# Optimization experiments

Hardware: AMD Instinct MI355X
Metric: run time of the kernel (lower is better)

The kernel has to match this reference:

```python
import jax, jax.numpy as jnp
import numpy as np

L, N, E, H = 2048, 4, 256, 4
D = E // H  # head_dim


def setup_inputs() -> dict:
    key = jax.random.key(0)
    ks = jax.random.split(key, 8)
    s = 1.0 / np.sqrt(E)
    return {
        "x": jax.random.normal(ks[0], (L, N, E), jnp.float32),
        "pos_emb": jax.random.normal(ks[1], (1, 2 * L - 1, E), jnp.float32),
        "in_proj_w": jax.random.normal(ks[2], (3 * E, E), jnp.float32) * s,
        "in_proj_b": jnp.zeros((3 * E,), jnp.float32),
        "pos_w": jax.random.normal(ks[3], (E, E), jnp.float32) * s,
        "pos_bias_u": jax.random.normal(ks[4], (H, D), jnp.float32) * s,
        "pos_bias_v": jax.random.normal(ks[5], (H, D), jnp.float32) * s,
        "out_proj_w": jax.random.normal(ks[6], (E, E), jnp.float32) * s,
        "out_proj_b": jnp.zeros((E,), jnp.float32),
    }


def _rel_shift(bd):
    # bd: (N, H, L, 2L-1) -> (N, H, L, L); out[...,i,j] = bd[...,i, L-1-i+j]
    l = bd.shape[2]
    idx = (l - 1) - jnp.arange(l)[:, None] + jnp.arange(l)[None, :]  # (L, L)
    return jnp.take_along_axis(bd, idx[None, None, :, :], axis=-1)


def reference(x, pos_emb, in_proj_w, in_proj_b, pos_w, pos_bias_u,
              pos_bias_v, out_proj_w, out_proj_b):
    scaling = 1.0 / jnp.sqrt(jnp.asarray(D, x.dtype))
    qkv = x @ in_proj_w.T + in_proj_b                # (L, N, 3E)
    q, k, v = jnp.split(qkv, 3, axis=-1)
    q = q * scaling
    # (L,N,E) -> (N,H,L,D)
    q = q.reshape(L, N, H, D).transpose(1, 2, 0, 3)
    k = k.reshape(L, N, H, D).transpose(1, 2, 0, 3)
    v = v.reshape(L, N, H, D).transpose(1, 2, 0, 3)
    # positional projection: (1, 2L-1, E) -> (H, 2L-1, D)
    p = (pos_emb @ pos_w.T).reshape(2 * L - 1, H, D).transpose(1, 0, 2)
    q_u = q + pos_bias_u[None, :, None, :]
    q_v = q + pos_bias_v[None, :, None, :]
    matrix_ac = jnp.einsum('bhld,bhsd->bhls', q_u, k)          # (N,H,L,L)
    matrix_bd = jnp.einsum('bhld,hnd->bhln', q_v, p)           # (N,H,L,2L-1)
    matrix_bd = _rel_shift(matrix_bd)                          # (N,H,L,L)
    scores = matrix_ac + matrix_bd
    attn = jax.nn.softmax(scores, axis=-1)
    out = jnp.einsum('bhls,bhsd->bhld', attn, v)               # (N,H,L,D)
    out = out.transpose(2, 0, 1, 3).reshape(L, N, E)
    return out @ out_proj_w.T + out_proj_b
```

## Files before the change

### kernel.cpp

```cpp
#include <hip/hip_runtime.h>
#include <math.h>
#include <stdint.h>


typedef __attribute__((ext_vector_type(8))) _Float16 half8;
typedef __attribute__((ext_vector_type(4))) float f32x4;
typedef unsigned short u16;
typedef unsigned int u32;

namespace {
constexpr int L_SEQ  = 2048;
constexpr int NB     = 4;
constexpr int EMB    = 256;
constexpr int NH     = 4;
constexpr int HD     = 64;
constexpr int P_ROWS = 2 * L_SEQ - 1;
}

__device__ __forceinline__ u16 f2h(float x) {
    _Float16 h = (_Float16)x;
    return __builtin_bit_cast(u16, h);
}
__device__ __forceinline__ u32 pk2(float a, float b) {
    return (u32)f2h(a) | ((u32)f2h(b) << 16);
}

__global__ __launch_bounds__(256, 2) void qkvpos_gemm(
        const float* __restrict__ x, const float* __restrict__ pos_emb,
        const float* __restrict__ in_w, const float* __restrict__ in_b,
        const float* __restrict__ pos_w,
        const float* __restrict__ u_bias, const float* __restrict__ v_bias,
        u16* __restrict__ quB, u16* __restrict__ qvB,
        u16* __restrict__ kB,  u16* __restrict__ vtB, u16* __restrict__ pB) {
    __shared__ __align__(16) u16 ws[64 * 256];
    __shared__ __align__(16) u16 scr[128 * 72];

    const int t    = threadIdx.x;
    const int lane = t & 63;
    const int w    = t >> 6;
    const int il   = lane & 15;
    const int g    = lane >> 4;

    const int logical = (blockIdx.x & 7) * 112 + (blockIdx.x >> 3);
    const bool isQKV = logical < 768;
    int mg, nt;
    const float *Ap, *W, *Wb;
    if (isQKV) { mg = logical / 12; nt = logical % 12; Ap = x;       W = in_w;  Wb = in_b; }
    else       { const int l2 = logical - 768;
                 mg = l2 >> 2;     nt = l2 & 3;      Ap = pos_emb; W = pos_w; Wb = nullptr; }
    const int m0 = mg * 128, n0 = nt * 64;

    {
        const int kc = (t & 31) * 8, rb_ = t >> 5;
        #pragma unroll
        for (int rr = 0; rr < 8; ++rr) {
            const int row = rb_ * 8 + rr;
            const float* wr = &W[(size_t)(n0 + row) * 256 + kc];
            float4 f0 = *(const float4*)&wr[0];
            float4 f1 = *(const float4*)&wr[4];
            *(uint4*)((char*)ws + row * 512 + ((kc * 2) ^ ((row & 7) << 4))) =
                make_uint4(pk2(f0.x, f0.y), pk2(f0.z, f0.w),
                           pk2(f1.x, f1.y), pk2(f1.z, f1.w));
        }
    }

    half8 bf0[8], bf1[8];
    {
        int r0 = m0 + w * 32 + il;
        int r1 = r0 + 16;
        if (!isQKV) { r0 = r0 > 4094 ? 4094 : r0; r1 = r1 > 4094 ? 4094 : r1; }
        const float* a0 = Ap + (size_t)r0 * 256;
        const float* a1 = Ap + (size_t)r1 * 256;
        #pragma unroll
        for (int c = 0; c < 8; ++c) {
            float4 f0 = *(const float4*)&a0[c * 32 + g * 8];
            float4 f1 = *(const float4*)&a0[c * 32 + g * 8 + 4];
            bf0[c] = __builtin_bit_cast(half8,
                make_uint4(pk2(f0.x, f0.y), pk2(f0.z, f0.w),
                           pk2(f1.x, f1.y), pk2(f1.z, f1.w)));
            float4 h0 = *(const float4*)&a1[c * 32 + g * 8];
            float4 h1 = *(const float4*)&a1[c * 32 + g * 8 + 4];
            bf1[c] = __builtin_bit_cast(half8,
                make_uint4(pk2(h0.x, h0.y), pk2(h0.z, h0.w),
                           pk2(h1.x, h1.y), pk2(h1.z, h1.w)));
        }
    }
    __syncthreads();

    f32x4 acc0[4] = {}, acc1[4] = {};
    __builtin_amdgcn_s_setprio(1);
    #pragma unroll
    for (int c = 0; c < 8; ++c) {
        #pragma unroll
        for (int jt = 0; jt < 4; ++jt) {
            const int row = jt * 16 + il;
            half8 af = *(const half8*)((const char*)ws + row * 512 +
                                       ((c * 64 + g * 16) ^ ((row & 7) << 4)));
            acc0[jt] = __builtin_amdgcn_mfma_f32_16x16x32_f16(af, bf0[c], acc0[jt], 0, 0, 0);
            acc1[jt] = __builtin_amdgcn_mfma_f32_16x16x32_f16(af, bf1[c], acc1[jt], 0, 0, 0);
        }
    }
    __builtin_amdgcn_s_setprio(0);

    float av[2][4][4];
    #pragma unroll
    for (int jt = 0; jt < 4; ++jt)
        #pragma unroll
        for (int r = 0; r < 4; ++r) {
            const float bb = Wb ? Wb[n0 + jt * 16 + g * 4 + r] : 0.f;
            av[0][jt][r] = acc0[jt][r] + bb;
            av[1][jt][r] = acc1[jt][r] + bb;
        }

    u16* scrw = scr + w * (32 * 72);
    const int rrd  = lane >> 1;
    const int base = (lane & 1) * 32;

    auto waveStore = [&](u16* dstBase, int hh, float scale, const float* bias,
                         bool qkvLayout) {
        #pragma unroll
        for (int s = 0; s < 2; ++s)
            #pragma unroll
            for (int jt = 0; jt < 4; ++jt) {
                const int d0 = jt * 16 + g * 4;
                float v0 = av[s][jt][0] * scale, v1 = av[s][jt][1] * scale;
                float v2 = av[s][jt][2] * scale, v3 = av[s][jt][3] * scale;
                if (bias) {
                    v0 += bias[hh * 64 + d0 + 0]; v1 += bias[hh * 64 + d0 + 1];
                    v2 += bias[hh * 64 + d0 + 2]; v3 += bias[hh * 64 + d0 + 3];
                }
                *(uint2*)&scrw[(s * 16 + il) * 72 + d0] = make_uint2(pk2(v0, v1), pk2(v2, v3));
            }
        uint4 q0 = *(const uint4*)&scrw[rrd * 72 + base + 0];
        uint4 q1 = *(const uint4*)&scrw[rrd * 72 + base + 8];
        uint4 q2 = *(const uint4*)&scrw[rrd * 72 + base + 16];
        uint4 q3 = *(const uint4*)&scrw[rrd * 72 + base + 24];
        const int mglob = m0 + w * 32 + rrd;
        if (qkvLayout) {
            const int i = mglob >> 2, b = mglob & 3;
            u16* dp = dstBase + (((size_t)(b * 4 + hh)) * 2048 + i) * 64 + base;
            *(uint4*)&dp[0] = q0; *(uint4*)&dp[8] = q1;
            *(uint4*)&dp[16] = q2; *(uint4*)&dp[24] = q3;
        } else if (mglob < P_ROWS) {
            u16* dp = dstBase + ((size_t)hh * P_ROWS + mglob) * 64 + base;
            *(uint4*)&dp[0] = q0; *(uint4*)&dp[8] = q1;
            *(uint4*)&dp[16] = q2; *(uint4*)&dp[24] = q3;
        }
    };

    if (isQKV) {
        const int seg = nt >> 2, h = nt & 3;
        if (seg == 0) {
            waveStore(quB, h, 0.125f, u_bias, true);
            waveStore(qvB, h, 0.125f, v_bias, true);
        } else if (seg == 1) {
            waveStore(kB, h, 1.f, nullptr, true);
        } else {
            #pragma unroll
            for (int s = 0; s < 2; ++s)
                #pragma unroll
                for (int jt = 0; jt < 4; ++jt)
                    *(uint2*)&scr[(w * 32 + s * 16 + il) * 72 + jt * 16 + g * 4] =
                        make_uint2(pk2(av[s][jt][0], av[s][jt][1]),
                                   pk2(av[s][jt][2], av[s][jt][3]));
            __syncthreads();
            const int b_ = w, d = lane;
            u32 pkx[16];
            #pragma unroll
            for (int z = 0; z < 16; ++z)
                pkx[z] = (u32)scr[((2 * z) * 4 + b_) * 72 + d] |
                         ((u32)scr[((2 * z + 1) * 4 + b_) * 72 + d] << 16);
            u16* dp = vtB + (((size_t)(b_ * 4 + h)) * 64 + d) * 2048 + mg * 32;
            *(uint4*)&dp[0]  = make_uint4(pkx[0],  pkx[1],  pkx[2],  pkx[3]);
            *(uint4*)&dp[8]  = make_uint4(pkx[4],  pkx[5],  pkx[6],  pkx[7]);
            *(uint4*)&dp[16] = make_uint4(pkx[8],  pkx[9],  pkx[10], pkx[11]);
            *(uint4*)&dp[24] = make_uint4(pkx[12], pkx[13], pkx[14], pkx[15]);
        }
    } else {
        waveStore(pB, nt, 1.f, nullptr, false);
    }
}

__global__ __launch_bounds__(256, 2) void out_gemm(
        const u16* __restrict__ attnb, const float* __restrict__ W,
        const float* __restrict__ Wb, float* __restrict__ outf) {
    __shared__ __align__(16) u16 ws[64 * 256];

    const int t    = threadIdx.x;
    const int lane = t & 63;
    const int w    = t >> 6;
    const int il   = lane & 15;
    const int g    = lane >> 4;

    const int logical = (blockIdx.x & 7) * 32 + (blockIdx.x >> 3);
    const int mg = logical >> 2, nt = logical & 3;
    const int m0 = mg * 128, n0 = nt * 64;

    {
        const int kc = (t & 31) * 8, rb_ = t >> 5;
        #pragma unroll
        for (int rr = 0; rr < 8; ++rr) {
            const int row = rb_ * 8 + rr;
            const float* wr = &W[(size_t)(n0 + row) * 256 + kc];
            float4 f0 = *(const float4*)&wr[0];
            float4 f1 = *(const float4*)&wr[4];
            *(uint4*)((char*)ws + row * 512 + ((kc * 2) ^ ((row & 7) << 4))) =
                make_uint4(pk2(f0.x, f0.y), pk2(f0.z, f0.w),
                           pk2(f1.x, f1.y), pk2(f1.z, f1.w));
        }
    }
    half8 bf0[8], bf1[8];
    {
        const u16* a0 = attnb + (size_t)(m0 + w * 32 + il) * 256;
        const u16* a1 = a0 + 16 * 256;
        #pragma unroll
        for (int c = 0; c < 8; ++c) {
            bf0[c] = *(const half8*)&a0[c * 32 + g * 8];
            bf1[c] = *(const half8*)&a1[c * 32 + g * 8];
        }
    }
    __syncthreads();

    f32x4 acc0[4] = {}, acc1[4] = {};
    __builtin_amdgcn_s_setprio(1);
    #pragma unroll
    for (int c = 0; c < 8; ++c) {
        #pragma unroll
        for (int jt = 0; jt < 4; ++jt) {
            const int row = jt * 16 + il;
            half8 af = *(const half8*)((const char*)ws + row * 512 +
                                       ((c * 64 + g * 16) ^ ((row & 7) << 4)));
            acc0[jt] = __builtin_amdgcn_mfma_f32_16x16x32_f16(af, bf0[c], acc0[jt], 0, 0, 0);
            acc1[jt] = __builtin_amdgcn_mfma_f32_16x16x32_f16(af, bf1[c], acc1[jt], 0, 0, 0);
        }
    }
    __builtin_amdgcn_s_setprio(0);

    #pragma unroll
    for (int s = 0; s < 2; ++s) {
        const int m_ = m0 + w * 32 + s * 16 + il;
        float* orow = &outf[(size_t)m_ * 256 + n0];
        #pragma unroll
        for (int jt = 0; jt < 4; ++jt) {
            const f32x4 a = s ? acc1[jt] : acc0[jt];
            *(float4*)&orow[jt * 16 + g * 4] = make_float4(
                a[0] + Wb[n0 + jt * 16 + g * 4 + 0],
                a[1] + Wb[n0 + jt * 16 + g * 4 + 1],
                a[2] + Wb[n0 + jt * 16 + g * 4 + 2],
                a[3] + Wb[n0 + jt * 16 + g * 4 + 3]);
        }
    }
}

__global__ __launch_bounds__(256, 2) void attn_mfma(
        const u16* __restrict__ quB, const u16* __restrict__ qvB,
        const u16* __restrict__ kB,  const u16* __restrict__ vtB,
        const u16* __restrict__ pB,  u16* __restrict__ attn_out) {
    __shared__ __align__(16) u16   k_s[64 * 64];
    __shared__ __align__(16) u16   v_s[64 * 64];
    __shared__ __align__(16) u16   p_s[128 * 64];
    __shared__ __align__(16) float bd_s[4][16 * 84];
    __shared__ __align__(16) u16   prob_s[4][16 * 64];

    const int t    = threadIdx.x;
    const int lane = t & 63;
    const int w    = t >> 6;
    const int il   = lane & 15;
    const int g    = lane >> 4;

    const int logical = ((blockIdx.x & 7) << 6) + (blockIdx.x >> 3);
    const int bh = logical >> 5;
    const int i0 = (logical & 31) * 64;
    const int b  = bh >> 2, h = bh & 3;

    half8 qu_f[2], qv_f[2];
    {
        const size_t qrow = ((size_t)bh * L_SEQ + i0 + w * 16 + il) * HD;
        qu_f[0] = *(const half8*)&quB[qrow + g * 8];
        qu_f[1] = *(const half8*)&quB[qrow + 32 + g * 8];
        qv_f[0] = *(const half8*)&qvB[qrow + g * 8];
        qv_f[1] = *(const half8*)&qvB[qrow + 32 + g * 8];
    }

    const int r0w = 48 - 16 * w;
    int krd[4][2], prd[5][2], pbrd[2], pwr[4];
    #pragma unroll
    for (int x4 = 0; x4 < 4; ++x4)
        #pragma unroll
        for (int c = 0; c < 2; ++c) {
            int row = x4 * 16 + il;
            krd[x4][c] = row * 128 + ((c * 64 + g * 16) ^ ((row & 7) << 4));
        }
    #pragma unroll
    for (int rt = 0; rt < 5; ++rt)
        #pragma unroll
        for (int c = 0; c < 2; ++c) {
            int row = r0w + rt * 16 + il;
            prd[rt][c] = row * 128 + ((c * 64 + g * 16) ^ ((row & 7) << 4));
        }
    #pragma unroll
    for (int c = 0; c < 2; ++c)
        pbrd[c] = il * 128 + ((c * 64 + g * 16) ^ ((il & 7) << 4));
    #pragma unroll
    for (int jt = 0; jt < 4; ++jt)
        pwr[jt] = il * 128 + (((jt * 16 + g * 4) * 2) ^ ((il & 7) << 4));
    const int bdwr = il * 84 + g * 4;
    const int bdrd = il * 83 + 15 + g * 4;

    f32x4 outacc[4] = {};
    float m_run = -INFINITY, l_run = 0.f;

    for (int kt = 0; kt < 32; ++kt) {
        const int j0 = kt * 64;
        const int nbase = 1984 - i0 + j0;
        __syncthreads();
        {
            const int rw = t >> 3;
            const int a  = t & 7;
            #pragma unroll
            for (int kr = 0; kr < 2; ++kr) {
                const int j = kr * 32 + rw;
                uint4 val = *(const uint4*)&kB[((size_t)bh * L_SEQ + j0 + j) * HD + a * 8];
                *(uint4*)((char*)k_s + (j * 128 + ((a * 16) ^ ((j & 7) << 4)))) = val;
            }
            #pragma unroll
            for (int vr = 0; vr < 2; ++vr) {
                const int d = vr * 32 + rw;
                uint4 val = *(const uint4*)&vtB[((size_t)bh * HD + d) * L_SEQ + j0 + a * 8];
                *(uint4*)((char*)v_s + (d * 128 + ((a * 16) ^ ((d & 7) << 4)))) = val;
            }
            #pragma unroll
            for (int pr = 0; pr < 4; ++pr) {
                const int r = pr * 32 + rw;
                int n = nbase + r; n = n > (P_ROWS - 1) ? (P_ROWS - 1) : n;
                uint4 val = *(const uint4*)&pB[((size_t)h * P_ROWS + n) * HD + a * 8];
                *(uint4*)((char*)p_s + (r * 128 + ((a * 16) ^ ((r & 7) << 4)))) = val;
            }
        }
        __syncthreads();

        __builtin_amdgcn_s_setprio(1);
        #pragma unroll
        for (int rt = 0; rt < 5; ++rt) {
            f32x4 acc = {};
            #pragma unroll
            for (int c = 0; c < 2; ++c) {
                half8 a = *(const half8*)((const char*)p_s + prd[rt][c]);
                acc = __builtin_amdgcn_mfma_f32_16x16x32_f16(a, qv_f[c], acc, 0, 0, 0);
            }
            *(f32x4*)&bd_s[w][bdwr + rt * 16] = acc;
        }
        __builtin_amdgcn_s_setprio(0);

        float sreg[16];
        __builtin_amdgcn_s_setprio(1);
        #pragma unroll
        for (int jt = 0; jt < 4; ++jt) {
            f32x4 acc = {};
            #pragma unroll
            for (int c = 0; c < 2; ++c) {
                half8 a = *(const half8*)((const char*)k_s + krd[jt][c]);
                acc = __builtin_amdgcn_mfma_f32_16x16x32_f16(a, qu_f[c], acc, 0, 0, 0);
            }
            #pragma unroll
            for (int tt = 0; tt < 4; ++tt)
                sreg[jt * 4 + tt] = acc[tt] + bd_s[w][bdrd + jt * 16 + tt];
        }
        __builtin_amdgcn_s_setprio(0);

        float mx = sreg[0];
        #pragma unroll
        for (int z = 1; z < 16; ++z) mx = fmaxf(mx, sreg[z]);
        mx = fmaxf(mx, __shfl_xor(mx, 16));
        mx = fmaxf(mx, __shfl_xor(mx, 32));
        const float m_new = fmaxf(m_run, mx);
        const float corr = __expf(m_run - m_new);
        float lsum = 0.f;
        #pragma unroll
        for (int z = 0; z < 16; ++z) { sreg[z] = __expf(sreg[z] - m_new); lsum += sreg[z]; }
        lsum += __shfl_xor(lsum, 16);
        lsum += __shfl_xor(lsum, 32);
        l_run = l_run * corr + lsum;
        m_run = m_new;
        #pragma unroll
        for (int dt = 0; dt < 4; ++dt) outacc[dt] *= corr;

        #pragma unroll
        for (int jt = 0; jt < 4; ++jt) {
            u32 lo = pk2(sreg[jt * 4 + 0], sreg[jt * 4 + 1]);
            u32 hi = pk2(sreg[jt * 4 + 2], sreg[jt * 4 + 3]);
            *(uint2*)((char*)&prob_s[w][0] + pwr[jt]) = make_uint2(lo, hi);
        }

        half8 pfrag[2];
        #pragma unroll
        for (int c = 0; c < 2; ++c)
            pfrag[c] = *(const half8*)((const char*)&prob_s[w][0] + pbrd[c]);
        __builtin_amdgcn_s_setprio(1);
        #pragma unroll
        for (int dt = 0; dt < 4; ++dt) {
            #pragma unroll
            for (int c = 0; c < 2; ++c) {
                half8 a = *(const half8*)((const char*)v_s + krd[dt][c]);
                outacc[dt] = __builtin_amdgcn_mfma_f32_16x16x32_f16(a, pfrag[c], outacc[dt], 0, 0, 0);
            }
        }
        __builtin_amdgcn_s_setprio(0);
    }

    const float inv = 1.f / l_run;
    const int m = (i0 + w * 16 + il) * NB + b;
    u16* orow = &attn_out[(size_t)m * EMB + h * HD];
    #pragma unroll
    for (int dt = 0; dt < 4; ++dt) {
        u32 lo = pk2(outacc[dt][0] * inv, outacc[dt][1] * inv);
        u32 hi = pk2(outacc[dt][2] * inv, outacc[dt][3] * inv);
        *(uint2*)&orow[dt * 16 + g * 4] = make_uint2(lo, hi);
    }
}

extern "C" void kernel_launch(void* const* d_in, const int* in_sizes, int n_in,
                              void* d_out, int out_size, void* d_ws, size_t ws_size,
                              hipStream_t stream) {
    const float* x        = (const float*)d_in[0];
    const float* pos_emb  = (const float*)d_in[1];
    const float* in_w     = (const float*)d_in[2];
    const float* in_b     = (const float*)d_in[3];
    const float* pos_w    = (const float*)d_in[4];
    const float* u_bias   = (const float*)d_in[5];
    const float* v_bias   = (const float*)d_in[6];
    const float* out_w    = (const float*)d_in[7];
    const float* out_b    = (const float*)d_in[8];
    float* out = (float*)d_out;

    u16* quB   = (u16*)d_ws;
    u16* qvB   = quB + (size_t)16 * L_SEQ * HD;
    u16* kB    = qvB + (size_t)16 * L_SEQ * HD;
    u16* vtB   = kB  + (size_t)16 * L_SEQ * HD;
    u16* pB    = vtB + (size_t)16 * L_SEQ * HD;
    u16* attnb = pB  + (size_t)NH * P_ROWS * HD;

    qkvpos_gemm<<<dim3(896), 256, 0, stream>>>(
        x, pos_emb, in_w, in_b, pos_w, u_bias, v_bias, quB, qvB, kB, vtB, pB);
    attn_mfma<<<dim3(512), 256, 0, stream>>>(quB, qvB, kB, vtB, pB, attnb);
    out_gemm<<<dim3(256), 256, 0, stream>>>(attnb, out_w, out_b, out);
}
```

Before: 171.4 us.

## Switch attention kernel to 32x32x16 MFMA with two 32-row waves per block

The attention kernel is rewritten to use 32x32x16 f16 MFMA tiles instead of 16x16x32. Each block now has 2 waves of 32 query rows rather than 4 waves of 16. The positional-score (BD) tile is computed in three 32-row chunks and re-gathered from shared memory to apply the relative shift, and the probability tile is repacked through shared memory for the PV product. The aim is fewer MFMA issues, less redundant P-tile work per query row, and better operand reuse. The cost is half the threads per block to stage K, V and P tiles, and possibly lower occupancy from larger register accumulators.

New measurement: 192.6 us. 12.3% more time.

```diff
diff --git a/kernel.cpp b/kernel.cpp
--- a/kernel.cpp
+++ b/kernel.cpp
@@ -5,6 +5,7 @@
 
 typedef __attribute__((ext_vector_type(8))) _Float16 half8;
 typedef __attribute__((ext_vector_type(4))) float f32x4;
+typedef __attribute__((ext_vector_type(16))) float f32x16;
 typedef unsigned short u16;
 typedef unsigned int u32;
 
@@ -252,170 +253,178 @@
     }
 }
 
-__global__ __launch_bounds__(256, 2) void attn_mfma(
+__global__ __launch_bounds__(128, 1) void attn_mfma(
         const u16* __restrict__ quB, const u16* __restrict__ qvB,
         const u16* __restrict__ kB,  const u16* __restrict__ vtB,
         const u16* __restrict__ pB,  u16* __restrict__ attn_out) {
     __shared__ __align__(16) u16   k_s[64 * 64];
     __shared__ __align__(16) u16   v_s[64 * 64];
     __shared__ __align__(16) u16   p_s[128 * 64];
-    __shared__ __align__(16) float bd_s[4][16 * 84];
-    __shared__ __align__(16) u16   prob_s[4][16 * 64];
+    __shared__ __align__(16) float bd_f[2 * 96 * 34];
+    __shared__ __align__(16) u32   pb_u[2 * 32 * 20];
 
     const int t    = threadIdx.x;
     const int lane = t & 63;
     const int w    = t >> 6;
-    const int il   = lane & 15;
-    const int g    = lane >> 4;
+    const int l31  = lane & 31;
+    const int hi   = lane >> 5;
+    const int hi4  = hi * 4;
 
     const int logical = ((blockIdx.x & 7) << 6) + (blockIdx.x >> 3);
     const int bh = logical >> 5;
     const int i0 = (logical & 31) * 64;
     const int b  = bh >> 2, h = bh & 3;
 
-    half8 qu_f[2], qv_f[2];
-    {
-        const size_t qrow = ((size_t)bh * L_SEQ + i0 + w * 16 + il) * HD;
-        qu_f[0] = *(const half8*)&quB[qrow + g * 8];
-        qu_f[1] = *(const half8*)&quB[qrow + 32 + g * 8];
-        qv_f[0] = *(const half8*)&qvB[qrow + g * 8];
-        qv_f[1] = *(const half8*)&qvB[qrow + 32 + g * 8];
-    }
-
-    const int r0w = 48 - 16 * w;
-    int krd[4][2], prd[5][2], pbrd[2], pwr[4];
-    #pragma unroll
-    for (int x4 = 0; x4 < 4; ++x4)
-        #pragma unroll
-        for (int c = 0; c < 2; ++c) {
-            int row = x4 * 16 + il;
-            krd[x4][c] = row * 128 + ((c * 64 + g * 16) ^ ((row & 7) << 4));
-        }
-    #pragma unroll
-    for (int rt = 0; rt < 5; ++rt)
-        #pragma unroll
-        for (int c = 0; c < 2; ++c) {
-            int row = r0w + rt * 16 + il;
-            prd[rt][c] = row * 128 + ((c * 64 + g * 16) ^ ((row & 7) << 4));
-        }
-    #pragma unroll
-    for (int c = 0; c < 2; ++c)
-        pbrd[c] = il * 128 + ((c * 64 + g * 16) ^ ((il & 7) << 4));
-    #pragma unroll
-    for (int jt = 0; jt < 4; ++jt)
-        pwr[jt] = il * 128 + (((jt * 16 + g * 4) * 2) ^ ((il & 7) << 4));
-    const int bdwr = il * 84 + g * 4;
-    const int bdrd = il * 83 + 15 + g * 4;
-
-    f32x4 outacc[4] = {};
+    int cx[4];
+    {
+        const int swz = (l31 & 7) << 4;
+        #pragma unroll
+        for (int ks = 0; ks < 4; ++ks)
+            cx[ks] = ((ks * 32 + hi * 16) ^ swz);
+    }
+    const int rowb = l31 * 128;
+
+    half8 qu_f[4], qv_f[4];
+    {
+        const size_t qrow = ((size_t)bh * L_SEQ + i0 + w * 32 + l31) * HD + hi * 8;
+        #pragma unroll
+        for (int ks = 0; ks < 4; ++ks) {
+            qu_f[ks] = *(const half8*)&quB[qrow + ks * 16];
+            qv_f[ks] = *(const half8*)&qvB[qrow + ks * 16];
+        }
+    }
+
+    const int W0 = w * 3264 + hi4 * 34 + l31;
+    const int G0 = w * 3264 + (31 - l31 + hi4) * 34 + l31;
+    const int PW = w * 640 + l31 * 20;
+    const int PRB = (w * 640 + l31 * 20) * 4 + hi * 16;
+
+    const int rw = t >> 3, a8 = t & 7;
+    const int wcol = (a8 * 16) ^ ((rw & 7) << 4);
+    const int R0 = 32 - 32 * w;
+    const int nb0 = 1984 - i0;
+
+    f32x16 out0 = {}, out1 = {};
     float m_run = -INFINITY, l_run = 0.f;
 
     for (int kt = 0; kt < 32; ++kt) {
         const int j0 = kt * 64;
-        const int nbase = 1984 - i0 + j0;
+        const int nb = nb0 + j0;
         __syncthreads();
-        {
-            const int rw = t >> 3;
-            const int a  = t & 7;
-            #pragma unroll
-            for (int kr = 0; kr < 2; ++kr) {
-                const int j = kr * 32 + rw;
-                uint4 val = *(const uint4*)&kB[((size_t)bh * L_SEQ + j0 + j) * HD + a * 8];
-                *(uint4*)((char*)k_s + (j * 128 + ((a * 16) ^ ((j & 7) << 4)))) = val;
+        #pragma unroll
+        for (int kr = 0; kr < 4; ++kr) {
+            const int j = kr * 16 + rw;
+            uint4 val = *(const uint4*)&kB[((size_t)bh * 2048 + j0 + j) * 64 + a8 * 8];
+            *(uint4*)((char*)k_s + j * 128 + wcol) = val;
+        }
+        #pragma unroll
+        for (int vr = 0; vr < 4; ++vr) {
+            const int d = vr * 16 + rw;
+            uint4 val = *(const uint4*)&vtB[((size_t)bh * 64 + d) * 2048 + j0 + a8 * 8];
+            *(uint4*)((char*)v_s + d * 128 + wcol) = val;
+        }
+        #pragma unroll
+        for (int pr = 0; pr < 8; ++pr) {
+            const int r = pr * 16 + rw;
+            int n = nb + r; n = n > (P_ROWS - 1) ? (P_ROWS - 1) : n; n = n < 0 ? 0 : n;
+            uint4 val = *(const uint4*)&pB[((size_t)h * P_ROWS + n) * 64 + a8 * 8];
+            *(uint4*)((char*)p_s + r * 128 + wcol) = val;
+        }
+        __syncthreads();
+
+        __builtin_amdgcn_s_setprio(1);
+        #pragma unroll
+        for (int rt = 0; rt < 3; ++rt) {
+            f32x16 bda = {};
+            #pragma unroll
+            for (int ks = 0; ks < 4; ++ks) {
+                half8 a = *(const half8*)((const char*)p_s + (R0 + rt * 32) * 128 + rowb + cx[ks]);
+                bda = __builtin_amdgcn_mfma_f32_32x32x16_f16(a, qv_f[ks], bda, 0, 0, 0);
             }
             #pragma unroll
-            for (int vr = 0; vr < 2; ++vr) {
-                const int d = vr * 32 + rw;
-                uint4 val = *(const uint4*)&vtB[((size_t)bh * HD + d) * L_SEQ + j0 + a * 8];
-                *(uint4*)((char*)v_s + (d * 128 + ((a * 16) ^ ((d & 7) << 4)))) = val;
-            }
-            #pragma unroll
-            for (int pr = 0; pr < 4; ++pr) {
-                const int r = pr * 32 + rw;
-                int n = nbase + r; n = n > (P_ROWS - 1) ? (P_ROWS - 1) : n;
-                uint4 val = *(const uint4*)&pB[((size_t)h * P_ROWS + n) * HD + a * 8];
-                *(uint4*)((char*)p_s + (r * 128 + ((a * 16) ^ ((r & 7) << 4)))) = val;
-            }
-        }
-        __syncthreads();
-
-        __builtin_amdgcn_s_setprio(1);
-        #pragma unroll
-        for (int rt = 0; rt < 5; ++rt) {
-            f32x4 acc = {};
-            #pragma unroll
-            for (int c = 0; c < 2; ++c) {
-                half8 a = *(const half8*)((const char*)p_s + prd[rt][c]);
-                acc = __builtin_amdgcn_mfma_f32_16x16x32_f16(a, qv_f[c], acc, 0, 0, 0);
-            }
-            *(f32x4*)&bd_s[w][bdwr + rt * 16] = acc;
+            for (int r = 0; r < 16; ++r)
+                bd_f[W0 + (rt * 32 + (r & 3) + 8 * (r >> 2)) * 34] = bda[r];
+        }
+
+        f32x16 s0 = {}, s1 = {};
+        #pragma unroll
+        for (int ks = 0; ks < 4; ++ks) {
+            half8 a0 = *(const half8*)((const char*)k_s + rowb + cx[ks]);
+            s0 = __builtin_amdgcn_mfma_f32_32x32x16_f16(a0, qu_f[ks], s0, 0, 0, 0);
+        }
+        #pragma unroll
+        for (int ks = 0; ks < 4; ++ks) {
+            half8 a1 = *(const half8*)((const char*)k_s + 32 * 128 + rowb + cx[ks]);
+            s1 = __builtin_amdgcn_mfma_f32_32x32x16_f16(a1, qu_f[ks], s1, 0, 0, 0);
         }
         __builtin_amdgcn_s_setprio(0);
 
-        float sreg[16];
-        __builtin_amdgcn_s_setprio(1);
-        #pragma unroll
-        for (int jt = 0; jt < 4; ++jt) {
-            f32x4 acc = {};
-            #pragma unroll
-            for (int c = 0; c < 2; ++c) {
-                half8 a = *(const half8*)((const char*)k_s + krd[jt][c]);
-                acc = __builtin_amdgcn_mfma_f32_16x16x32_f16(a, qu_f[c], acc, 0, 0, 0);
-            }
-            #pragma unroll
-            for (int tt = 0; tt < 4; ++tt)
-                sreg[jt * 4 + tt] = acc[tt] + bd_s[w][bdrd + jt * 16 + tt];
-        }
-        __builtin_amdgcn_s_setprio(0);
-
-        float mx = sreg[0];
-        #pragma unroll
-        for (int z = 1; z < 16; ++z) mx = fmaxf(mx, sreg[z]);
-        mx = fmaxf(mx, __shfl_xor(mx, 16));
+        #pragma unroll
+        for (int r = 0; r < 16; ++r) {
+            const int off = ((r & 3) + 8 * (r >> 2)) * 34;
+            s0[r] += bd_f[G0 + off];
+            s1[r] += bd_f[G0 + 1088 + off];
+        }
+
+        float mx = s0[0];
+        #pragma unroll
+        for (int r = 1; r < 16; ++r) mx = fmaxf(mx, s0[r]);
+        #pragma unroll
+        for (int r = 0; r < 16; ++r) mx = fmaxf(mx, s1[r]);
         mx = fmaxf(mx, __shfl_xor(mx, 32));
         const float m_new = fmaxf(m_run, mx);
         const float corr = __expf(m_run - m_new);
         float lsum = 0.f;
         #pragma unroll
-        for (int z = 0; z < 16; ++z) { sreg[z] = __expf(sreg[z] - m_new); lsum += sreg[z]; }
-        lsum += __shfl_xor(lsum, 16);
+        for (int r = 0; r < 16; ++r) { s0[r] = __expf(s0[r] - m_new); lsum += s0[r]; }
+        #pragma unroll
+        for (int r = 0; r < 16; ++r) { s1[r] = __expf(s1[r] - m_new); lsum += s1[r]; }
         lsum += __shfl_xor(lsum, 32);
         l_run = l_run * corr + lsum;
         m_run = m_new;
         #pragma unroll
-        for (int dt = 0; dt < 4; ++dt) outacc[dt] *= corr;
-
-        #pragma unroll
-        for (int jt = 0; jt < 4; ++jt) {
-            u32 lo = pk2(sreg[jt * 4 + 0], sreg[jt * 4 + 1]);
-            u32 hi = pk2(sreg[jt * 4 + 2], sreg[jt * 4 + 3]);
-            *(uint2*)((char*)&prob_s[w][0] + pwr[jt]) = make_uint2(lo, hi);
-        }
-
-        half8 pfrag[2];
-        #pragma unroll
-        for (int c = 0; c < 2; ++c)
-            pfrag[c] = *(const half8*)((const char*)&prob_s[w][0] + pbrd[c]);
-        __builtin_amdgcn_s_setprio(1);
-        #pragma unroll
-        for (int dt = 0; dt < 4; ++dt) {
-            #pragma unroll
-            for (int c = 0; c < 2; ++c) {
-                half8 a = *(const half8*)((const char*)v_s + krd[dt][c]);
-                outacc[dt] = __builtin_amdgcn_mfma_f32_16x16x32_f16(a, pfrag[c], outacc[dt], 0, 0, 0);
+        for (int r = 0; r < 16; ++r) { out0[r] *= corr; out1[r] *= corr; }
+
+        #pragma unroll
+        for (int jt = 0; jt < 2; ++jt) {
+            #pragma unroll
+            for (int k4 = 0; k4 < 4; ++k4) {
+                const float e0 = jt ? s1[k4 * 4 + 0] : s0[k4 * 4 + 0];
+                const float e1 = jt ? s1[k4 * 4 + 1] : s0[k4 * 4 + 1];
+                const float e2 = jt ? s1[k4 * 4 + 2] : s0[k4 * 4 + 2];
+                const float e3 = jt ? s1[k4 * 4 + 3] : s0[k4 * 4 + 3];
+                *(uint2*)&pb_u[PW + k4 * 4 + hi * 2] = make_uint2(pk2(e0, e1), pk2(e2, e3));
             }
-        }
-        __builtin_amdgcn_s_setprio(0);
+            half8 pf0 = *(const half8*)((const char*)pb_u + PRB);
+            half8 pf1 = *(const half8*)((const char*)pb_u + PRB + 32);
+            __builtin_amdgcn_s_setprio(1);
+            {
+                half8 va = *(const half8*)((const char*)v_s + rowb + cx[jt * 2 + 0]);
+                out0 = __builtin_amdgcn_mfma_f32_32x32x16_f16(va, pf0, out0, 0, 0, 0);
+                half8 vb = *(const half8*)((const char*)v_s + rowb + cx[jt * 2 + 1]);
+                out0 = __builtin_amdgcn_mfma_f32_32x32x16_f16(vb, pf1, out0, 0, 0, 0);
+                half8 vc = *(const half8*)((const char*)v_s + 32 * 128 + rowb + cx[jt * 2 + 0]);
+                out1 = __builtin_amdgcn_mfma_f32_32x32x16_f16(vc, pf0, out1, 0, 0, 0);
+                half8 vd = *(const half8*)((const char*)v_s + 32 * 128 + rowb + cx[jt * 2 + 1]);
+                out1 = __builtin_amdgcn_mfma_f32_32x32x16_f16(vd, pf1, out1, 0, 0, 0);
+            }
+            __builtin_amdgcn_s_setprio(0);
+        }
     }
 
     const float inv = 1.f / l_run;
-    const int m = (i0 + w * 16 + il) * NB + b;
+    const int i = i0 + w * 32 + l31;
+    const int m = i * NB + b;
     u16* orow = &attn_out[(size_t)m * EMB + h * HD];
     #pragma unroll
-    for (int dt = 0; dt < 4; ++dt) {
-        u32 lo = pk2(outacc[dt][0] * inv, outacc[dt][1] * inv);
-        u32 hi = pk2(outacc[dt][2] * inv, outacc[dt][3] * inv);
-        *(uint2*)&orow[dt * 16 + g * 4] = make_uint2(lo, hi);
+    for (int k4 = 0; k4 < 4; ++k4) {
+        const int d0 = k4 * 8 + hi4;
+        *(uint2*)&orow[d0] = make_uint2(
+            pk2(out0[k4 * 4 + 0] * inv, out0[k4 * 4 + 1] * inv),
+            pk2(out0[k4 * 4 + 2] * inv, out0[k4 * 4 + 3] * inv));
+        *(uint2*)&orow[32 + d0] = make_uint2(
+            pk2(out1[k4 * 4 + 0] * inv, out1[k4 * 4 + 1] * inv),
+            pk2(out1[k4 * 4 + 2] * inv, out1[k4 * 4 + 3] * inv));
     }
 }
 
@@ -442,6 +451,6 @@
 
     qkvpos_gemm<<<dim3(896), 256, 0, stream>>>(
         x, pos_emb, in_w, in_b, pos_w, u_bias, v_bias, quB, qvB, kB, vtB, pB);
-    attn_mfma<<<dim3(512), 256, 0, stream>>>(quB, qvB, kB, vtB, pB, attnb);
+    attn_mfma<<<dim3(512), 128, 0, stream>>>(quB, qvB, kB, vtB, pB, attnb);
     out_gemm<<<dim3(256), 256, 0, stream>>>(attnb, out_w, out_b, out);
 }
```
